# Kernel tuning notes

Hardware: AMD Instinct MI355X
Metric: run time of the kernel (lower is better)

Reference implementation:

```python
import jax, jax.numpy as jnp
import numpy as np

EPS = 1e-06
NUM_HEADS = 16
HEAD_DIM = 72
HIDDEN = 1152
N = 4096


def _rms_norm(x, weight=None):
    # x: [..., head_dim]; computed in fp32 as in the torch reference
    xf = x.astype(jnp.float32)
    ms = jnp.mean(xf * xf, axis=-1, keepdims=True) + EPS
    y = xf * jax.lax.rsqrt(ms)
    if weight is not None:
        y = y * weight.astype(jnp.float32)
    return y.astype(x.dtype)


def _rotate_half(x):
    h = x.shape[-1] // 2
    return jnp.concatenate([-x[..., h:], x[..., :h]], axis=-1)


def _apply_2d_rope(x, cos, sin):
    # x: [n, H, head_dim]; cos/sin: [n, head_dim] (first half dim-0 freqs, second half dim-1)
    hd = x.shape[-1]
    x1, x2 = x[..., : hd // 2], x[..., hd // 2 :]
    c1, c2 = jnp.split(cos, 2, axis=-1)
    s1, s2 = jnp.split(sin, 2, axis=-1)

    def ap(xp, c, s):
        c = c[:, None, :]  # broadcast over heads (unsqueeze_dim=1)
        s = s[:, None, :]
        return xp * c + _rotate_half(xp) * s

    return jnp.concatenate([ap(x1, c1, s1), ap(x2, c2, s2)], axis=-1)


def setup_inputs() -> dict:
    key = jax.random.key(0)
    ks = jax.random.split(key, 8)
    hidden_states = jax.random.normal(ks[0], (N, HIDDEN), dtype=jnp.float32)
    cos = jax.random.uniform(ks[1], (N, HEAD_DIM), dtype=jnp.float32, minval=-1.0, maxval=1.0)
    sin = jax.random.uniform(ks[2], (N, HEAD_DIM), dtype=jnp.float32, minval=-1.0, maxval=1.0)
    proj = NUM_HEADS * HEAD_DIM
    Wq = jax.random.normal(ks[3], (HIDDEN, proj), dtype=jnp.float32) * 0.02
    Wk = jax.random.normal(ks[4], (HIDDEN, proj), dtype=jnp.float32) * 0.02
    Wv = jax.random.normal(ks[5], (HIDDEN, proj), dtype=jnp.float32) * 0.02
    Wo = jax.random.normal(ks[6], (proj, HIDDEN), dtype=jnp.float32) * 0.02
    q_scale = jnp.ones((HEAD_DIM,), dtype=jnp.float32)
    k_scale = jnp.ones((HEAD_DIM,), dtype=jnp.float32)
    return {
        "hidden_states": hidden_states, "cos": cos, "sin": sin,
        "Wq": Wq, "Wk": Wk, "Wv": Wv, "Wo": Wo,
        "q_scale": q_scale, "k_scale": k_scale,
    }


def reference(hidden_states, cos, sin, Wq, Wk, Wv, Wo, q_scale, k_scale):
    n = hidden_states.shape[0]
    xq = (hidden_states @ Wq).reshape(n, NUM_HEADS, HEAD_DIM)
    xk = (hidden_states @ Wk).reshape(n, NUM_HEADS, HEAD_DIM)
    xv = (hidden_states @ Wv).reshape(n, NUM_HEADS, HEAD_DIM)
    xq = _rms_norm(xq, q_scale)
    xk = _rms_norm(xk, k_scale)
    xv = _rms_norm(xv)  # no scale
    xq = _apply_2d_rope(xq, cos, sin)
    xk = _apply_2d_rope(xk, cos, sin)
    # eager bidirectional attention, scale = 1.0
    attn = jnp.einsum("nhd,mhd->hnm", xq, xk)  # [H, n, n]
    attn = jax.nn.softmax(attn.astype(jnp.float32), axis=-1).astype(xq.dtype)
    out = jnp.einsum("hnm,mhd->nhd", attn, xv)  # [n, H, d]
    out = out.reshape(n, NUM_HEADS * HEAD_DIM)
    return out @ Wo
```

## Files before the change

kernel.cpp:

```cpp
#include <hip/hip_runtime.h>
#include <stdint.h>

typedef unsigned short u16;
typedef __bf16 bf16x8 __attribute__((ext_vector_type(8)));
typedef float f32x4 __attribute__((ext_vector_type(4)));
typedef __attribute__((address_space(1))) const unsigned int as1_u32;
typedef __attribute__((address_space(3))) unsigned int as3_u32;

#define SEQ 4096
#define HID 1152
#define NH 16
#define HD 72

__device__ __forceinline__ void gload_lds16(const void* g, void* l) {
  __builtin_amdgcn_global_load_lds((as1_u32*)g, (as3_u32*)l, 16, 0, 0);
}
__device__ __forceinline__ u16 f2bf(float f) {
  __bf16 h = (__bf16)f;
  return __builtin_bit_cast(u16, h);
}
__device__ __forceinline__ float bf2f(u16 u) {
  unsigned int x = ((unsigned int)u) << 16;
  return __builtin_bit_cast(float, x);
}

__global__ void cvt_x(const float* __restrict__ X, u16* __restrict__ Xb, int n4) {
  int i = blockIdx.x * blockDim.x + threadIdx.x;
  if (i < n4) {
    float4 v = *(const float4*)(X + (size_t)i * 4);
    unsigned int lo = f2bf(v.x) | ((unsigned int)f2bf(v.y) << 16);
    unsigned int hi = f2bf(v.z) | ((unsigned int)f2bf(v.w) << 16);
    *(uint2*)(Xb + (size_t)i * 4) = make_uint2(lo, hi);
  }
}

__global__ void transpose_w(const float* __restrict__ Wq, const float* __restrict__ Wk,
                            const float* __restrict__ Wv, const float* __restrict__ Wo,
                            u16* __restrict__ Wt, u16* __restrict__ Wot) {
  __shared__ __align__(16) float t[32][33];
  int z = blockIdx.z;
  const float* src = (z == 0) ? Wq : (z == 1) ? Wk : (z == 2) ? Wv : Wo;
  u16* dst = (z < 3) ? (Wt + (size_t)z * HID * HID) : Wot;
  int tx = threadIdx.x & 31, ty = threadIdx.x >> 5;
  int c0 = blockIdx.x * 32, r0 = blockIdx.y * 32;
#pragma unroll
  for (int i = 0; i < 4; i++)
    t[ty + i * 8][tx] = src[(size_t)(r0 + ty + i * 8) * HID + c0 + tx];
  __syncthreads();
#pragma unroll
  for (int i = 0; i < 4; i++)
    dst[(size_t)(c0 + ty + i * 8) * HID + r0 + tx] = f2bf(t[tx][ty + i * 8]);
}

template <int OUTBF16>
__global__ __launch_bounds__(256, 2) void gemm_bt(const u16* __restrict__ A,
                                                  const u16* __restrict__ Bt,
                                                  void* __restrict__ Cout,
                                                  int M, int N, int K) {
  __shared__ __align__(16) u16 lds[2][2][128 * 64];
  const int tid = threadIdx.x;
  const int wave = tid >> 6, lane = tid & 63;
  const int l15 = lane & 15, l4 = lane >> 4;
  const size_t bm = (size_t)blockIdx.x * 128, bn = (size_t)blockIdx.y * 128;
  const int wm = (wave >> 1) * 64, wn = (wave & 1) * 64;
  const int nt = K >> 6;

  f32x4 acc[4][4] = {};

  auto stage = [&](int buf, int kt) {
    const int k0 = kt << 6;
#pragma unroll
    for (int r = 0; r < 4; r++) {
      int idx = (r << 8) + tid;
      int m = idx >> 3, j = idx & 7;
      int js = j ^ (m & 7);
      void* ldsA = (void*)&lds[buf][0][(size_t)((r << 8) + (wave << 6)) * 8];
      void* ldsB = (void*)&lds[buf][1][(size_t)((r << 8) + (wave << 6)) * 8];
      gload_lds16(A + (bm + m) * (size_t)K + k0 + js * 8, ldsA);
      gload_lds16(Bt + (bn + m) * (size_t)K + k0 + js * 8, ldsB);
    }
  };

  stage(0, 0);
  for (int t = 0; t < nt; t++) {
    __syncthreads();
    if (t + 1 < nt) stage((t + 1) & 1, t + 1);
    const u16* As = &lds[t & 1][0][0];
    const u16* Bs = &lds[t & 1][1][0];
#pragma unroll
    for (int kk = 0; kk < 2; kk++) {
      bf16x8 af[4], bfr[4];
      int slot = (kk << 2) + l4;
#pragma unroll
      for (int mi = 0; mi < 4; mi++) {
        int m = wm + (mi << 4) + l15;
        af[mi] = *(const bf16x8*)&As[m * 64 + ((slot ^ (m & 7)) << 3)];
      }
#pragma unroll
      for (int ni = 0; ni < 4; ni++) {
        int n = wn + (ni << 4) + l15;
        bfr[ni] = *(const bf16x8*)&Bs[n * 64 + ((slot ^ (n & 7)) << 3)];
      }
#pragma unroll
      for (int mi = 0; mi < 4; mi++)
#pragma unroll
        for (int ni = 0; ni < 4; ni++)
          acc[mi][ni] = __builtin_amdgcn_mfma_f32_16x16x32_bf16(af[mi], bfr[ni], acc[mi][ni], 0, 0, 0);
    }
  }

#pragma unroll
  for (int mi = 0; mi < 4; mi++)
#pragma unroll
    for (int ni = 0; ni < 4; ni++)
#pragma unroll
      for (int r = 0; r < 4; r++) {
        size_t m = bm + wm + (mi << 4) + (l4 << 2) + r;
        size_t n = bn + wn + (ni << 4) + l15;
        if (OUTBF16)
          ((u16*)Cout)[m * N + n] = f2bf(acc[mi][ni][r]);
        else
          ((float*)Cout)[m * N + n] = acc[mi][ni][r];
      }
}

__global__ __launch_bounds__(256, 2) void norm_rope(
    const u16* __restrict__ C1, const float* __restrict__ cosv,
    const float* __restrict__ sinv, const float* __restrict__ qsc,
    const float* __restrict__ ksc, u16* __restrict__ Qp, u16* __restrict__ Kp,
    u16* __restrict__ Vt) {
  __shared__ __align__(16) u16 in_t[32 * 224];
  __shared__ __align__(16) u16 qo[32 * 96];
  __shared__ __align__(16) u16 ko[32 * 96];
  __shared__ __align__(16) u16 vo[80 * 48];
  const int tid = threadIdx.x;
  const int h = blockIdx.y;
  const int n0 = blockIdx.x * 32;

#pragma unroll
  for (int k = 0; k < 4; k++) {
    int g = tid + k * 256;
    if (g < 864) {
      int row = g / 27, j = g - row * 27;
      int seg = j / 9, c = (j - seg * 9) * 8;
      const u16* src = C1 + (size_t)(n0 + row) * 3456 + seg * 1152 + h * HD + c;
      *(uint4*)&in_t[row * 224 + j * 8] = *(const uint4*)src;
    }
  }
  __syncthreads();

  const int r = tid >> 3, p = tid & 7;
  float sq = 0, sk = 0, sv = 0;
  auto acc8 = [&](int off, float& s) {
    uint4 v = *(const uint4*)&in_t[r * 224 + off];
    unsigned int vv[4] = {v.x, v.y, v.z, v.w};
#pragma unroll
    for (int q = 0; q < 4; q++) {
      float a = bf2f((u16)(vv[q] & 0xffff));
      float b = bf2f((u16)(vv[q] >> 16));
      s += a * a + b * b;
    }
  };
  acc8(0 + p * 8, sq);
  acc8(72 + p * 8, sk);
  acc8(144 + p * 8, sv);
  if (p == 0) { acc8(64, sq); acc8(136, sk); acc8(208, sv); }
#pragma unroll
  for (int m = 1; m < 8; m <<= 1) {
    sq += __shfl_xor(sq, m);
    sk += __shfl_xor(sk, m);
    sv += __shfl_xor(sv, m);
  }
  const float rq = rsqrtf(sq * (1.0f / 72.0f) + 1e-6f);
  const float rk = rsqrtf(sk * (1.0f / 72.0f) + 1e-6f);
  const float rv = rsqrtf(sv * (1.0f / 72.0f) + 1e-6f);

#pragma unroll
  for (int u = 0; u < 5; u++) {
    int ti = p + (u << 3);
    if (ti < 36) {
      int i1 = ti + ((ti >= 18) ? 18 : 0);
      int i2 = i1 + 18;
      const float* cb = cosv + (size_t)(n0 + r) * HD;
      const float* sb = sinv + (size_t)(n0 + r) * HD;
      float c1 = cb[i1], c2 = cb[i2], s1 = sb[i1], s2 = sb[i2];
      float q1 = bf2f(in_t[r * 224 + i1]) * rq * qsc[i1];
      float q2 = bf2f(in_t[r * 224 + i2]) * rq * qsc[i2];
      float k1 = bf2f(in_t[r * 224 + 72 + i1]) * rk * ksc[i1];
      float k2 = bf2f(in_t[r * 224 + 72 + i2]) * rk * ksc[i2];
      qo[r * 96 + i1] = f2bf(q1 * c1 - q2 * s1);
      qo[r * 96 + i2] = f2bf(q2 * c2 + q1 * s2);
      ko[r * 96 + i1] = f2bf(k1 * c1 - k2 * s1);
      ko[r * 96 + i2] = f2bf(k2 * c2 + k1 * s2);
    }
  }
#pragma unroll
  for (int u = 0; u < 9; u++) {
    int d = p * 9 + u;
    vo[d * 48 + r] = f2bf(bf2f(in_t[r * 224 + 144 + d]) * rv);
  }
  if (p < 3) {
    uint4 z = make_uint4(0, 0, 0, 0);
    *(uint4*)&qo[r * 96 + (9 + p) * 8] = z;
    *(uint4*)&ko[r * 96 + (9 + p) * 8] = z;
  }
  if (tid < 32) {
    int d = 72 + (tid >> 2), g = tid & 3;
    *(uint4*)&vo[d * 48 + g * 8] = make_uint4(0, 0, 0, 0);
  }
  __syncthreads();

#pragma unroll
  for (int k = 0; k < 2; k++) {
    int g = tid + k * 256;
    if (g < 384) {
      int row = g / 12, j = g - row * 12;
      *(uint4*)(Qp + ((size_t)h * SEQ + n0 + row) * 96 + j * 8) = *(const uint4*)&qo[row * 96 + j * 8];
      *(uint4*)(Kp + ((size_t)h * SEQ + n0 + row) * 128 + j * 8) = *(const uint4*)&ko[row * 96 + j * 8];
    }
  }
#pragma unroll
  for (int k = 0; k < 2; k++) {
    int g = tid + k * 256;
    if (g < 320) {
      int d = g >> 2, j = g & 3;
      *(uint4*)(Vt + ((size_t)h * 80 + d) * SEQ + n0 + j * 8) = *(const uint4*)&vo[d * 48 + j * 8];
    }
  }
}

__global__ __launch_bounds__(512, 4) void attn(const u16* __restrict__ Qp,
                                               const u16* __restrict__ Kp,
                                               const u16* __restrict__ Vt,
                                               u16* __restrict__ AO) {
  __shared__ __align__(16) u16 Ks[2][64 * 128];
  __shared__ __align__(16) u16 Vs[2][80 * 64];
  __shared__ __align__(16) u16 Ps[8][16 * 64];
  const int tid = threadIdx.x;
  const int wave = tid >> 6, lane = tid & 63;
  const int l15 = lane & 15, l4 = lane >> 4;

  const int bid = blockIdx.x + (blockIdx.y << 5);
  const int h = ((bid & 7) << 1) | ((bid >> 3) & 1);
  const int qt = bid >> 4;
  const int q0 = qt * 128 + wave * 16;

  bf16x8 bq[3];
  const u16* qbase = Qp + ((size_t)h * SEQ + q0 + l15) * 96;
#pragma unroll
  for (int kk = 0; kk < 3; kk++) bq[kk] = *(const bf16x8*)(qbase + kk * 32 + l4 * 8);

  f32x4 acc[5] = {};
  float mi_ = -1e30f, li_ = 0.0f;

  auto stage = [&](int buf, int k0) {
    {
      int m = tid >> 4, j = tid & 15;
      int js = j ^ (m & 15);
      gload_lds16(Kp + ((size_t)h * SEQ + k0 + m) * 128 + js * 8,
                  (void*)&Ks[buf][(size_t)(wave << 6) * 8]);
      int g2 = tid + 512;
      int m2 = g2 >> 4, j2 = g2 & 15;
      int js2 = j2 ^ (m2 & 15);
      gload_lds16(Kp + ((size_t)h * SEQ + k0 + m2) * 128 + js2 * 8,
                  (void*)&Ks[buf][(size_t)(512 + (wave << 6)) * 8]);
    }
    {
      int d = tid >> 3, j = tid & 7;
      int js = j ^ (d & 7);
      gload_lds16(Vt + ((size_t)h * 80 + d) * SEQ + k0 + js * 8,
                  (void*)&Vs[buf][(size_t)(wave << 6) * 8]);
      if (wave < 2) {
        int g2 = tid + 512;
        int d2 = g2 >> 3, j2 = g2 & 7;
        int js2 = j2 ^ (d2 & 7);
        gload_lds16(Vt + ((size_t)h * 80 + d2) * SEQ + k0 + js2 * 8,
                    (void*)&Vs[buf][(size_t)(512 + (wave << 6)) * 8]);
      }
    }
  };

  stage(0, 0);
  for (int t = 0; t < 64; t++) {
    __syncthreads();
    if (t < 63) stage((t + 1) & 1, (t + 1) * 64);
    const u16* Kb = Ks[t & 1];
    const u16* Vb = Vs[t & 1];

    f32x4 s[4] = {};
    __builtin_amdgcn_s_setprio(1);
#pragma unroll
    for (int kk = 0; kk < 3; kk++) {
      int slot = (kk << 2) + l4;
      bf16x8 ak[4];
#pragma unroll
      for (int nf = 0; nf < 4; nf++) {
        int row = (nf << 4) + l15;
        ak[nf] = *(const bf16x8*)&Kb[row * 128 + ((slot ^ l15) << 3)];
      }
#pragma unroll
      for (int nf = 0; nf < 4; nf++)
        s[nf] = __builtin_amdgcn_mfma_f32_16x16x32_bf16(ak[nf], bq[kk], s[nf], 0, 0, 0);
    }
    __builtin_amdgcn_s_setprio(0);

    float v0 = fmaxf(fmaxf(s[0][0], s[0][1]), fmaxf(s[0][2], s[0][3]));
    float v1 = fmaxf(fmaxf(s[1][0], s[1][1]), fmaxf(s[1][2], s[1][3]));
    float v2 = fmaxf(fmaxf(s[2][0], s[2][1]), fmaxf(s[2][2], s[2][3]));
    float v3 = fmaxf(fmaxf(s[3][0], s[3][1]), fmaxf(s[3][2], s[3][3]));
    float v = fmaxf(fmaxf(v0, v1), fmaxf(v2, v3));
    v = fmaxf(v, __shfl_xor(v, 16));
    v = fmaxf(v, __shfl_xor(v, 32));
    float mnew = fmaxf(mi_, v);
    float scl = __expf(mi_ - mnew);
    mi_ = mnew;
    float rsum = 0.0f;
#pragma unroll
    for (int nf = 0; nf < 4; nf++) {
      ushort4 pk;
      float p0 = __expf(s[nf][0] - mnew);
      float p1 = __expf(s[nf][1] - mnew);
      float p2 = __expf(s[nf][2] - mnew);
      float p3 = __expf(s[nf][3] - mnew);
      rsum += (p0 + p1) + (p2 + p3);
      pk.x = f2bf(p0); pk.y = f2bf(p1); pk.z = f2bf(p2); pk.w = f2bf(p3);
      int gs = ((nf << 2) + l4) ^ ((l15 & 7) << 1);
      *(ushort4*)&Ps[wave][l15 * 64 + gs * 4] = pk;
    }
    li_ = li_ * scl + rsum;

#pragma unroll
    for (int r = 0; r < 4; r++) {
      float sr = __shfl(scl, (l4 << 2) + r);
#pragma unroll
      for (int ni = 0; ni < 5; ni++) acc[ni][r] *= sr;
    }

    __builtin_amdgcn_s_setprio(1);
#pragma unroll
    for (int kk = 0; kk < 2; kk++) {
      int gb = ((kk << 3) + (l4 << 1)) ^ ((l15 & 7) << 1);
      bf16x8 pa = *(const bf16x8*)&Ps[wave][l15 * 64 + gb * 4];
      int slot = (kk << 2) + l4;
#pragma unroll
      for (int ni = 0; ni < 5; ni++) {
        int d = (ni << 4) + l15;
        bf16x8 bv = *(const bf16x8*)&Vb[d * 64 + ((slot ^ (d & 7)) << 3)];
        acc[ni] = __builtin_amdgcn_mfma_f32_16x16x32_bf16(pa, bv, acc[ni], 0, 0, 0);
      }
    }
    __builtin_amdgcn_s_setprio(0);
  }

  li_ += __shfl_xor(li_, 16);
  li_ += __shfl_xor(li_, 32);
#pragma unroll
  for (int r = 0; r < 4; r++) {
    float inv = 1.0f / __shfl(li_, (l4 << 2) + r);
    int q = q0 + (l4 << 2) + r;
#pragma unroll
    for (int ni = 0; ni < 5; ni++) {
      int d = (ni << 4) + l15;
      if (d < HD) AO[(size_t)q * HID + h * HD + d] = f2bf(acc[ni][r] * inv);
    }
  }
}

extern "C" void kernel_launch(void* const* d_in, const int* in_sizes, int n_in,
                              void* d_out, int out_size, void* d_ws, size_t ws_size,
                              hipStream_t stream) {
  const float* X = (const float*)d_in[0];
  const float* cosv = (const float*)d_in[1];
  const float* sinv = (const float*)d_in[2];
  const float* Wq = (const float*)d_in[3];
  const float* Wk = (const float*)d_in[4];
  const float* Wv = (const float*)d_in[5];
  const float* Wo = (const float*)d_in[6];
  const float* qsc = (const float*)d_in[7];
  const float* ksc = (const float*)d_in[8];
  float* out = (float*)d_out;

  uint8_t* ws = (uint8_t*)d_ws;
  u16* Xb  = (u16*)(ws);
  u16* Wt  = (u16*)(ws + 9437184);
  u16* Wot = (u16*)(ws + 17399808);
  u16* C1  = (u16*)(ws + 20054016);
  u16* Qp  = (u16*)(ws + 48365568);
  u16* Kp  = (u16*)(ws + 60948480);
  u16* Vt  = (u16*)(ws + 77725696);
  u16* AO  = Xb;

  cvt_x<<<4608, 256, 0, stream>>>(X, Xb, (SEQ * HID) / 4);
  transpose_w<<<dim3(36, 36, 4), 256, 0, stream>>>(Wq, Wk, Wv, Wo, Wt, Wot);
  gemm_bt<1><<<dim3(32, 27), 256, 0, stream>>>(Xb, Wt, (void*)C1, SEQ, 3456, HID);
  norm_rope<<<dim3(128, 16), 256, 0, stream>>>(C1, cosv, sinv, qsc, ksc, Qp, Kp, Vt);
  attn<<<dim3(32, 16), 512, 0, stream>>>(Qp, Kp, Vt, AO);
  gemm_bt<0><<<dim3(32, 9), 256, 0, stream>>>(AO, Wot, (void*)out, SEQ, HID, HID);
}
```

Baseline: 299.5 us.

## Double attention KV tile to 128 keys and skip redundant softmax rescale

The attention kernel now processes 128 keys per iteration instead of 64. This halves the number of barriers and stage calls and changes the LDS layout and swizzles for the K, V and P buffers. It also skips the accumulator and row-sum rescale whenever no row maximum increases, and simplifies staging address math with incrementing pointers. LDS use roughly doubles and launch bounds drop to 1 block per SM, which can reduce occupancy.

```diff
diff --git a/kernel.cpp b/kernel.cpp
--- a/kernel.cpp
+++ b/kernel.cpp
@@ -229,13 +229,13 @@
   }
 }
 
-__global__ __launch_bounds__(512, 4) void attn(const u16* __restrict__ Qp,
+__global__ __launch_bounds__(512, 1) void attn(const u16* __restrict__ Qp,
                                                const u16* __restrict__ Kp,
                                                const u16* __restrict__ Vt,
                                                u16* __restrict__ AO) {
-  __shared__ __align__(16) u16 Ks[2][64 * 128];
-  __shared__ __align__(16) u16 Vs[2][80 * 64];
-  __shared__ __align__(16) u16 Ps[8][16 * 64];
+  __shared__ __align__(16) u16 Ks[2][128 * 128];
+  __shared__ __align__(16) u16 Vs[2][80 * 128];
+  __shared__ __align__(16) u16 Ps[8][16 * 128];
   const int tid = threadIdx.x;
   const int wave = tid >> 6, lane = tid & 63;
   const int l15 = lane & 15, l4 = lane >> 4;
@@ -253,99 +253,95 @@
   f32x4 acc[5] = {};
   float mi_ = -1e30f, li_ = 0.0f;
 
-  auto stage = [&](int buf, int k0) {
-    {
-      int m = tid >> 4, j = tid & 15;
-      int js = j ^ (m & 15);
-      gload_lds16(Kp + ((size_t)h * SEQ + k0 + m) * 128 + js * 8,
-                  (void*)&Ks[buf][(size_t)(wave << 6) * 8]);
-      int g2 = tid + 512;
-      int m2 = g2 >> 4, j2 = g2 & 15;
-      int js2 = j2 ^ (m2 & 15);
-      gload_lds16(Kp + ((size_t)h * SEQ + k0 + m2) * 128 + js2 * 8,
-                  (void*)&Ks[buf][(size_t)(512 + (wave << 6)) * 8]);
-    }
-    {
-      int d = tid >> 3, j = tid & 7;
-      int js = j ^ (d & 7);
-      gload_lds16(Vt + ((size_t)h * 80 + d) * SEQ + k0 + js * 8,
-                  (void*)&Vs[buf][(size_t)(wave << 6) * 8]);
-      if (wave < 2) {
-        int g2 = tid + 512;
-        int d2 = g2 >> 3, j2 = g2 & 7;
-        int js2 = j2 ^ (d2 & 7);
-        gload_lds16(Vt + ((size_t)h * 80 + d2) * SEQ + k0 + js2 * 8,
-                    (void*)&Vs[buf][(size_t)(512 + (wave << 6)) * 8]);
-      }
-    }
+  const int r0 = (wave << 2) + l4;
+  const int js = l15 ^ (r0 & 15);
+  const u16* kS = Kp + ((size_t)h * SEQ + r0) * 128 + js * 8;
+  const u16* vS = Vt + ((size_t)h * 80 + r0) * SEQ + js * 8;
+
+  auto stage = [&](int buf) {
+#pragma unroll
+    for (int i = 0; i < 4; i++)
+      gload_lds16(kS + (size_t)(i * 32) * 128,
+                  (void*)&Ks[buf][(size_t)((i << 9) + (wave << 6)) * 8]);
+#pragma unroll
+    for (int i = 0; i < 2; i++)
+      gload_lds16(vS + (size_t)(i * 32) * SEQ,
+                  (void*)&Vs[buf][(size_t)((i << 9) + (wave << 6)) * 8]);
+    if (wave < 4)
+      gload_lds16(vS + (size_t)64 * SEQ,
+                  (void*)&Vs[buf][(size_t)(1024 + (wave << 6)) * 8]);
+    kS += 128 * 128;
+    vS += 128;
   };
 
-  stage(0, 0);
-  for (int t = 0; t < 64; t++) {
+  stage(0);
+#pragma unroll 2
+  for (int t = 0; t < 32; t++) {
     __syncthreads();
-    if (t < 63) stage((t + 1) & 1, (t + 1) * 64);
+    if (t < 31) stage((t + 1) & 1);
     const u16* Kb = Ks[t & 1];
     const u16* Vb = Vs[t & 1];
 
-    f32x4 s[4] = {};
+    f32x4 s[8];
+#pragma unroll
+    for (int nf = 0; nf < 8; nf++) s[nf] = f32x4{0.f, 0.f, 0.f, 0.f};
     __builtin_amdgcn_s_setprio(1);
 #pragma unroll
     for (int kk = 0; kk < 3; kk++) {
       int slot = (kk << 2) + l4;
-      bf16x8 ak[4];
-#pragma unroll
-      for (int nf = 0; nf < 4; nf++) {
+#pragma unroll
+      for (int nf = 0; nf < 8; nf++) {
         int row = (nf << 4) + l15;
-        ak[nf] = *(const bf16x8*)&Kb[row * 128 + ((slot ^ l15) << 3)];
-      }
-#pragma unroll
-      for (int nf = 0; nf < 4; nf++)
-        s[nf] = __builtin_amdgcn_mfma_f32_16x16x32_bf16(ak[nf], bq[kk], s[nf], 0, 0, 0);
+        bf16x8 ak = *(const bf16x8*)&Kb[row * 128 + ((slot ^ l15) << 3)];
+        s[nf] = __builtin_amdgcn_mfma_f32_16x16x32_bf16(ak, bq[kk], s[nf], 0, 0, 0);
+      }
     }
     __builtin_amdgcn_s_setprio(0);
 
-    float v0 = fmaxf(fmaxf(s[0][0], s[0][1]), fmaxf(s[0][2], s[0][3]));
-    float v1 = fmaxf(fmaxf(s[1][0], s[1][1]), fmaxf(s[1][2], s[1][3]));
-    float v2 = fmaxf(fmaxf(s[2][0], s[2][1]), fmaxf(s[2][2], s[2][3]));
-    float v3 = fmaxf(fmaxf(s[3][0], s[3][1]), fmaxf(s[3][2], s[3][3]));
-    float v = fmaxf(fmaxf(v0, v1), fmaxf(v2, v3));
-    v = fmaxf(v, __shfl_xor(v, 16));
-    v = fmaxf(v, __shfl_xor(v, 32));
-    float mnew = fmaxf(mi_, v);
-    float scl = __expf(mi_ - mnew);
-    mi_ = mnew;
+    float vmax = -1e30f;
+#pragma unroll
+    for (int nf = 0; nf < 8; nf++)
+      vmax = fmaxf(vmax, fmaxf(fmaxf(s[nf][0], s[nf][1]), fmaxf(s[nf][2], s[nf][3])));
+    vmax = fmaxf(vmax, __shfl_xor(vmax, 16));
+    vmax = fmaxf(vmax, __shfl_xor(vmax, 32));
+    if (!__all(vmax <= mi_)) {
+      float mnew = fmaxf(mi_, vmax);
+      float scl = __expf(mi_ - mnew);
+      mi_ = mnew;
+      li_ *= scl;
+#pragma unroll
+      for (int r = 0; r < 4; r++) {
+        float sr = __shfl(scl, (l4 << 2) + r);
+#pragma unroll
+        for (int ni = 0; ni < 5; ni++) acc[ni][r] *= sr;
+      }
+    }
+    const float mcur = mi_;
     float rsum = 0.0f;
 #pragma unroll
-    for (int nf = 0; nf < 4; nf++) {
+    for (int nf = 0; nf < 8; nf++) {
       ushort4 pk;
-      float p0 = __expf(s[nf][0] - mnew);
-      float p1 = __expf(s[nf][1] - mnew);
-      float p2 = __expf(s[nf][2] - mnew);
-      float p3 = __expf(s[nf][3] - mnew);
+      float p0 = __expf(s[nf][0] - mcur);
+      float p1 = __expf(s[nf][1] - mcur);
+      float p2 = __expf(s[nf][2] - mcur);
+      float p3 = __expf(s[nf][3] - mcur);
       rsum += (p0 + p1) + (p2 + p3);
       pk.x = f2bf(p0); pk.y = f2bf(p1); pk.z = f2bf(p2); pk.w = f2bf(p3);
       int gs = ((nf << 2) + l4) ^ ((l15 & 7) << 1);
-      *(ushort4*)&Ps[wave][l15 * 64 + gs * 4] = pk;
-    }
-    li_ = li_ * scl + rsum;
-
-#pragma unroll
-    for (int r = 0; r < 4; r++) {
-      float sr = __shfl(scl, (l4 << 2) + r);
-#pragma unroll
-      for (int ni = 0; ni < 5; ni++) acc[ni][r] *= sr;
-    }
+      *(ushort4*)&Ps[wave][l15 * 128 + gs * 4] = pk;
+    }
+    li_ += rsum;
 
     __builtin_amdgcn_s_setprio(1);
 #pragma unroll
-    for (int kk = 0; kk < 2; kk++) {
+    for (int kk = 0; kk < 4; kk++) {
       int gb = ((kk << 3) + (l4 << 1)) ^ ((l15 & 7) << 1);
-      bf16x8 pa = *(const bf16x8*)&Ps[wave][l15 * 64 + gb * 4];
+      bf16x8 pa = *(const bf16x8*)&Ps[wave][l15 * 128 + gb * 4];
       int slot = (kk << 2) + l4;
 #pragma unroll
       for (int ni = 0; ni < 5; ni++) {
         int d = (ni << 4) + l15;
-        bf16x8 bv = *(const bf16x8*)&Vb[d * 64 + ((slot ^ (d & 7)) << 3)];
+        bf16x8 bv = *(const bf16x8*)&Vb[d * 128 + ((slot ^ l15) << 3)];
         acc[ni] = __builtin_amdgcn_mfma_f32_16x16x32_bf16(pa, bv, acc[ni], 0, 0, 0);
       }
     }
```

Measured after the change: 325.0 us. +8.5%, slower.
